# Performance work log

Measured on AMD Instinct MI355X. Metric: run time of the kernel, lower is better.

The kernel has to match this reference:

```python
import jax, jax.numpy as jnp
from jax import lax
import numpy as np

B, C, H, W = 16, 64, 256, 256
K = 7


def setup_inputs() -> dict:
    key = jax.random.key(0)
    kx, kk = jax.random.split(key)
    x = jax.random.normal(kx, (B, C, H, W), dtype=jnp.float32)
    kernel = jax.random.normal(kk, (K, K), dtype=jnp.float32)
    return {"x": x, "kernel": kernel}


def reference(x, kernel):
    # Depthwise conv: every (b, ch) slice convolved with the SAME [K,K] kernel.
    # scipy-style true convolution => flip the kernel, 'same' padding.
    c = x.shape[1]
    kflip = jnp.flip(kernel, axis=(0, 1))
    w = jnp.tile(kflip[None, None], (c, 1, 1, 1))  # [C,1,K,K]
    y = lax.conv_general_dilated(
        x, w,
        window_strides=(1, 1),
        padding='SAME',
        feature_group_count=c,
        dimension_numbers=('NCHW', 'OIHW', 'NCHW'),
    )
    # mish(y) = y * tanh(softplus(y))
    return y * jnp.tanh(jax.nn.softplus(y))
```

## Files before the change

### kernel.cpp

```cpp
#include <hip/hip_runtime.h>


#define HW 256
#define RING 40
#define PITCH 272
#define TPB 8

typedef _Float16 f16x8 __attribute__((ext_vector_type(8)));
typedef float    f32x4 __attribute__((ext_vector_type(4)));
typedef __fp16   h2    __attribute__((ext_vector_type(2)));
union U32H2 { unsigned u; h2 h; };
union BFU   { uint4 u; f16x8 h; };

__device__ __forceinline__ float mish_f(float y) {
    float t = __expf(y);
    float u = 1.0f + t;
    float d = __fmaf_rn(u, u, 1.0f);
    return y * (1.0f - __fdividef(2.0f, d));
}

__global__ __launch_bounds__(256)
__attribute__((amdgpu_waves_per_eu(2, 7)))
void dwconv7_mish_ring6(const float* __restrict__ x,
                        const float* __restrict__ kern,
                        float* __restrict__ out) {
    __shared__ __align__(16) _Float16 ring[RING * PITCH];
    unsigned* lds_B = (unsigned*)ring;

    const int tid  = threadIdx.x;
    const int lane = tid & 63;
    const int w    = tid >> 6;
    const int lrow = lane & 15;
    const int lk   = lane >> 4;
    const int c0   = w << 6;

    const int bid   = blockIdx.x;
    const int plane = bid >> 1;
    const int r0    = (bid & 1) << 7;

    const float* __restrict__ xp = x + (size_t)plane * (HW * HW);
    float* __restrict__ op = out + (size_t)plane * (HW * HW);

    float kf[49];
    #pragma unroll
    for (int i = 0; i < 49; ++i) {
        int p = i / 7, q = i - p * 7;
        kf[i] = __int_as_float(__builtin_amdgcn_readfirstlane(
                    __float_as_int(kern[(6 - p) * 7 + (6 - q)])));
    }

    {
        const int j  = tid >> 4;
        const int kw = tid & 15;
        #pragma unroll
        for (int p = 0; p < 7; ++p) {
            const int d0 = 2 * kw - j - 5;
            const int d1 = d0 + 1;
            float v0 = 0.f, v1 = 0.f;
            #pragma unroll
            for (int q = 0; q < 7; ++q) {
                v0 = (d0 == q) ? kf[p * 7 + q] : v0;
                v1 = (d1 == q) ? kf[p * 7 + q] : v1;
            }
            U32H2 u; u.h = __builtin_amdgcn_cvt_pkrtz(v0, v1);
            lds_B[p * 256 + tid] = u.u;
        }
    }
    __syncthreads();

    f16x8 bfrag[7];
    #pragma unroll
    for (int p = 0; p < 7; ++p) {
        BFU bu;
        bu.u = ((const uint4*)lds_B)[(p << 6) + (lrow << 2) + lk];
        bfrag[p] = bu.h;
    }
    __syncthreads();

    if (tid < 160) {
        int row = tid >> 2, q = tid & 3;
        ((uint2*)ring)[row * 68 + (q < 2 ? q : 64 + q)] = make_uint2(0u, 0u);
    }

    #pragma unroll
    for (int i = 0; i < 6; ++i) {
        const int row = w + 4 * i;
        if (row < 22) {
            const int gr = r0 - 3 + row;
            const int slot = (gr + RING) % RING;
            float4 f = make_float4(0.f, 0.f, 0.f, 0.f);
            if ((unsigned)gr < (unsigned)HW)
                f = *(const float4*)(xp + (gr << 8) + 4 * lane);
            U32H2 a, b;
            a.h = __builtin_amdgcn_cvt_pkrtz(f.x, f.y);
            b.h = __builtin_amdgcn_cvt_pkrtz(f.z, f.w);
            ((uint2*)ring)[slot * 68 + 2 + lane] = make_uint2(a.u, b.u);
        }
    }
    __syncthreads();

    float4 rf[4];

    #pragma unroll 1
    for (int t = 0; t < TPB; ++t) {
        const int W = r0 + (t << 4);

        if (t + 1 < TPB) {
            #pragma unroll
            for (int i = 0; i < 4; ++i) {
                const int gr = W + 19 + w + 4 * i;
                rf[i] = make_float4(0.f, 0.f, 0.f, 0.f);
                if (gr < HW)
                    rf[i] = *(const float4*)(xp + (gr << 8) + 4 * lane);
            }
        }
        __builtin_amdgcn_sched_barrier(0);

        const int b0 = (W + 37) % RING;
        int sa[7];
        #pragma unroll
        for (int p = 0; p < 7; ++p) {
            int s = b0 + lrow + p;
            s -= (s >= RING) ? RING : 0;
            sa[p] = s * PITCH;
        }
        #pragma unroll
        for (int t4 = 0; t4 < 4; ++t4) {
            f32x4 acc = {0.f, 0.f, 0.f, 0.f};
            #pragma unroll
            for (int p = 0; p < 7; ++p) {
                f16x8 a = *(const f16x8*)(ring + sa[p] + c0 + 16 * t4 + 8 * lk);
                acc = __builtin_amdgcn_mfma_f32_16x16x32_f16(a, bfrag[p], acc,
                                                             0, 0, 0);
            }
            const int col = c0 + 16 * t4 + lrow;
            const int rb  = W + (lk << 2);
            op[(rb + 0) * HW + col] = mish_f(acc[0]);
            op[(rb + 1) * HW + col] = mish_f(acc[1]);
            op[(rb + 2) * HW + col] = mish_f(acc[2]);
            op[(rb + 3) * HW + col] = mish_f(acc[3]);
        }
        __builtin_amdgcn_sched_barrier(0);

        if (t + 1 < TPB) {
            #pragma unroll
            for (int i = 0; i < 4; ++i) {
                const int gr = W + 19 + w + 4 * i;
                const int slot = gr % RING;
                U32H2 a, b;
                a.h = __builtin_amdgcn_cvt_pkrtz(rf[i].x, rf[i].y);
                b.h = __builtin_amdgcn_cvt_pkrtz(rf[i].z, rf[i].w);
                ((uint2*)ring)[slot * 68 + 2 + lane] = make_uint2(a.u, b.u);
            }
        }

        asm volatile("s_waitcnt lgkmcnt(0)\n\ts_barrier" ::: "memory");
        __builtin_amdgcn_sched_barrier(0);
    }
}

extern "C" void kernel_launch(void* const* d_in, const int* in_sizes, int n_in,
                              void* d_out, int out_size, void* d_ws, size_t ws_size,
                              hipStream_t stream) {
    const float* x = (const float*)d_in[0];
    const float* k = (const float*)d_in[1];
    float* out = (float*)d_out;

    dim3 grid(2 * 16 * 64, 1, 1);
    dim3 block(256);
    dwconv7_mish_ring6<<<grid, block, 0, stream>>>(x, k, out);
}
```

Before: 114.9 us.

## Give each wave a private LDS ring with halo columns to drop block barriers

Replaces the shared block-wide LDS ring with four per-wave rings, each holding the wave's 64-column strip plus an 8-column halo on each side. Each wave loads its own halo rows, with clamped addresses and masking in place of branches, so the per-iteration s_barrier goes away and only a wave-local lgkmcnt wait remains. The cost is redundant global loads of halo columns, 25% more row loads per wave, and a different LDS footprint. This relies on wave-lockstep ordering of LDS writes and reads within a wave.

```diff
diff --git a/kernel.cpp b/kernel.cpp
--- a/kernel.cpp
+++ b/kernel.cpp
@@ -3,7 +3,7 @@
 
 #define HW 256
 #define RING 40
-#define PITCH 272
+#define WPITCH 80
 #define TPB 8
 
 typedef _Float16 f16x8 __attribute__((ext_vector_type(8)));
@@ -21,11 +21,10 @@
 
 __global__ __launch_bounds__(256)
 __attribute__((amdgpu_waves_per_eu(2, 7)))
-void dwconv7_mish_ring6(const float* __restrict__ x,
+void dwconv7_mish_wring(const float* __restrict__ x,
                         const float* __restrict__ kern,
                         float* __restrict__ out) {
-    __shared__ __align__(16) _Float16 ring[RING * PITCH];
-    unsigned* lds_B = (unsigned*)ring;
+    __shared__ __align__(16) _Float16 rings[4][RING * WPITCH];
 
     const int tid  = threadIdx.x;
     const int lane = tid & 63;
@@ -40,6 +39,8 @@
 
     const float* __restrict__ xp = x + (size_t)plane * (HW * HW);
     float* __restrict__ op = out + (size_t)plane * (HW * HW);
+
+    unsigned* lds_B = (unsigned*)&rings[0][0];
 
     float kf[49];
     #pragma unroll
@@ -77,29 +78,49 @@
     }
     __syncthreads();
 
-    if (tid < 160) {
-        int row = tid >> 2, q = tid & 3;
-        ((uint2*)ring)[row * 68 + (q < 2 ? q : 64 + q)] = make_uint2(0u, 0u);
-    }
-
-    #pragma unroll
-    for (int i = 0; i < 6; ++i) {
-        const int row = w + 4 * i;
-        if (row < 22) {
-            const int gr = r0 - 3 + row;
+    _Float16* ring = rings[w];
+
+    int ro_[7]; int gcc_[7]; unsigned cm_[7];
+    #pragma unroll
+    for (int i = 0; i < 7; ++i) {
+        int idx = lane + (i << 6);
+        int r = idx / 20, g = idx - 20 * r;
+        ro_[i] = r;
+        int gc = c0 - 8 + 4 * g;
+        cm_[i]  = ((unsigned)gc <= (unsigned)(HW - 4)) ? 0xffffffffu : 0u;
+        gcc_[i] = gc < 0 ? 0 : (gc > HW - 4 ? HW - 4 : gc);
+    }
+
+    #pragma unroll
+    for (int i = 0; i < 7; ++i) {
+        if (i < 6 || lane < 56) {
+            const int gr  = r0 - 3 + ro_[i];
+            const int grc = gr < 0 ? 0 : (gr > HW - 1 ? HW - 1 : gr);
+            float4 f = *(const float4*)(xp + (grc << 8) + gcc_[i]);
+            const unsigned m = ((unsigned)gr < (unsigned)HW) ? cm_[i] : 0u;
+            U32H2 a, b;
+            a.h = __builtin_amdgcn_cvt_pkrtz(
+                      __uint_as_float(__float_as_uint(f.x) & m),
+                      __uint_as_float(__float_as_uint(f.y) & m));
+            b.h = __builtin_amdgcn_cvt_pkrtz(
+                      __uint_as_float(__float_as_uint(f.z) & m),
+                      __uint_as_float(__float_as_uint(f.w) & m));
             const int slot = (gr + RING) % RING;
-            float4 f = make_float4(0.f, 0.f, 0.f, 0.f);
-            if ((unsigned)gr < (unsigned)HW)
-                f = *(const float4*)(xp + (gr << 8) + 4 * lane);
-            U32H2 a, b;
-            a.h = __builtin_amdgcn_cvt_pkrtz(f.x, f.y);
-            b.h = __builtin_amdgcn_cvt_pkrtz(f.z, f.w);
-            ((uint2*)ring)[slot * 68 + 2 + lane] = make_uint2(a.u, b.u);
-        }
-    }
-    __syncthreads();
-
-    float4 rf[4];
+            ((uint2*)ring)[slot * 20 + (lane + (i << 6)) - 20 * ro_[i]] =
+                make_uint2(a.u, b.u);
+        }
+    }
+
+    int sm_[5];
+    #pragma unroll
+    for (int i = 0; i < 5; ++i) sm_[i] = (r0 + 19 + ro_[i]) % RING;
+    int go_[5];
+    #pragma unroll
+    for (int i = 0; i < 5; ++i) go_[i] = (lane + (i << 6)) - 20 * ro_[i];
+
+    int b0 = (r0 + 37) % RING;
+
+    float4 rf[5];
 
     #pragma unroll 1
     for (int t = 0; t < TPB; ++t) {
@@ -107,29 +128,30 @@
 
         if (t + 1 < TPB) {
             #pragma unroll
-            for (int i = 0; i < 4; ++i) {
-                const int gr = W + 19 + w + 4 * i;
-                rf[i] = make_float4(0.f, 0.f, 0.f, 0.f);
-                if (gr < HW)
-                    rf[i] = *(const float4*)(xp + (gr << 8) + 4 * lane);
-            }
-        }
-        __builtin_amdgcn_sched_barrier(0);
-
-        const int b0 = (W + 37) % RING;
+            for (int i = 0; i < 5; ++i) {
+                const int gr  = W + 19 + ro_[i];
+                const int grc = gr > HW - 1 ? HW - 1 : gr;
+                rf[i] = *(const float4*)(xp + (grc << 8) + gcc_[i]);
+            }
+        }
+        __builtin_amdgcn_sched_barrier(0);
+
+        asm volatile("s_waitcnt lgkmcnt(0)" ::: "memory");
+        __builtin_amdgcn_sched_barrier(0);
+
         int sa[7];
         #pragma unroll
         for (int p = 0; p < 7; ++p) {
             int s = b0 + lrow + p;
             s -= (s >= RING) ? RING : 0;
-            sa[p] = s * PITCH;
+            sa[p] = s * WPITCH;
         }
         #pragma unroll
         for (int t4 = 0; t4 < 4; ++t4) {
             f32x4 acc = {0.f, 0.f, 0.f, 0.f};
             #pragma unroll
             for (int p = 0; p < 7; ++p) {
-                f16x8 a = *(const f16x8*)(ring + sa[p] + c0 + 16 * t4 + 8 * lk);
+                f16x8 a = *(const f16x8*)(ring + sa[p] + 16 * t4 + 8 * lk);
                 acc = __builtin_amdgcn_mfma_f32_16x16x32_f16(a, bfrag[p], acc,
                                                              0, 0, 0);
             }
@@ -144,17 +166,24 @@
 
         if (t + 1 < TPB) {
             #pragma unroll
-            for (int i = 0; i < 4; ++i) {
-                const int gr = W + 19 + w + 4 * i;
-                const int slot = gr % RING;
+            for (int i = 0; i < 5; ++i) {
+                const int gr = W + 19 + ro_[i];
+                const unsigned m = ((unsigned)gr < (unsigned)HW) ? cm_[i] : 0u;
                 U32H2 a, b;
-                a.h = __builtin_amdgcn_cvt_pkrtz(rf[i].x, rf[i].y);
-                b.h = __builtin_amdgcn_cvt_pkrtz(rf[i].z, rf[i].w);
-                ((uint2*)ring)[slot * 68 + 2 + lane] = make_uint2(a.u, b.u);
-            }
-        }
-
-        asm volatile("s_waitcnt lgkmcnt(0)\n\ts_barrier" ::: "memory");
+                a.h = __builtin_amdgcn_cvt_pkrtz(
+                          __uint_as_float(__float_as_uint(rf[i].x) & m),
+                          __uint_as_float(__float_as_uint(rf[i].y) & m));
+                b.h = __builtin_amdgcn_cvt_pkrtz(
+                          __uint_as_float(__float_as_uint(rf[i].z) & m),
+                          __uint_as_float(__float_as_uint(rf[i].w) & m));
+                ((uint2*)ring)[sm_[i] * 20 + go_[i]] = make_uint2(a.u, b.u);
+                sm_[i] += 16;
+                sm_[i] -= (sm_[i] >= RING) ? RING : 0;
+            }
+        }
+
+        b0 += 16;
+        b0 -= (b0 >= RING) ? RING : 0;
         __builtin_amdgcn_sched_barrier(0);
     }
 }
@@ -168,5 +197,5 @@
 
     dim3 grid(2 * 16 * 64, 1, 1);
     dim3 block(256);
-    dwconv7_mish_ring6<<<grid, block, 0, stream>>>(x, k, out);
+    dwconv7_mish_wring<<<grid, block, 0, stream>>>(x, k, out);
 }
```

After: 120.3 us. 4.8% more time.
